# Performance work log

Hardware: AMD Instinct MI355X
Metric: run time of the kernel (lower is better)

The kernel has to match this reference:

```python
import jax, jax.numpy as jnp
import numpy as np

B, NPG, CIN, D, C, H, E, MAXN = 128, 1000, 16, 128, 12, 4, 640000, 1001
N = B * NPG
DH = D // H
NL = 3


def _ln(x, w, b):
    m = x.mean(-1, keepdims=True)
    v = ((x - m) ** 2).mean(-1, keepdims=True)
    return (x - m) * jax.lax.rsqrt(v + 1e-5) * w + b


def _mha(q_in, k_in, v_in, qkv_w, qkv_b, out_w, out_b, pad=None):
    # torch nn.MultiheadAttention with packed in_proj: rows [0:D]=Q, [D:2D]=K, [2D:3D]=V
    Tq, Tk = q_in.shape[1], k_in.shape[1]
    q = (q_in @ qkv_w[:D].T + qkv_b[:D]).reshape(-1, Tq, H, DH)
    k = (k_in @ qkv_w[D:2 * D].T + qkv_b[D:2 * D]).reshape(-1, Tk, H, DH)
    v = (v_in @ qkv_w[2 * D:].T + qkv_b[2 * D:]).reshape(-1, Tk, H, DH)
    s = jnp.einsum('bqhd,bkhd->bhqk', q, k) / np.sqrt(DH).astype(np.float32)
    if pad is not None:
        s = jnp.where(pad[:, None, None, :], jnp.float32(-1e30), s)
    a = jax.nn.softmax(s, axis=-1)
    o = jnp.einsum('bhqk,bkhd->bqhd', a, v).reshape(-1, Tq, D)
    return o @ out_w.T + out_b


def setup_inputs():
    key = jax.random.key(0)
    ks = iter(jax.random.split(key, 48))
    def nrm(shape, s=0.05):
        return jax.random.normal(next(ks), shape, jnp.float32) * s
    inp = {
        'x': nrm((N, CIN), 1.0),
        'edge_index': jax.random.randint(next(ks), (2, E), 0, N, dtype=jnp.int32),
        'batch': (jnp.arange(N, dtype=jnp.int32) // NPG),
        'in_w': nrm((D, CIN)), 'in_b': nrm((D,)),
        'gcn_w': nrm((NL, D, D)), 'gcn_b': nrm((NL, D)),
        'ln_w': jnp.ones((NL, D), jnp.float32), 'ln_b': jnp.zeros((NL, D), jnp.float32),
        'cq': nrm((C, D), 1.0),
        'sa_qkv_w': nrm((3 * D, D)), 'sa_qkv_b': nrm((3 * D,)),
        'sa_out_w': nrm((D, D)), 'sa_out_b': nrm((D,)),
        'ca_qkv_w': nrm((3 * D, D)), 'ca_qkv_b': nrm((3 * D,)),
        'ca_out_w': nrm((D, D)), 'ca_out_b': nrm((D,)),
        'n1_w': jnp.ones((D,), jnp.float32), 'n1_b': jnp.zeros((D,), jnp.float32),
        'n2_w': jnp.ones((D,), jnp.float32), 'n2_b': jnp.zeros((D,), jnp.float32),
        'n3_w': jnp.ones((D,), jnp.float32), 'n3_b': jnp.zeros((D,), jnp.float32),
        'ff1_w': nrm((4 * D, D)), 'ff1_b': nrm((4 * D,)),
        'ff2_w': nrm((D, 4 * D)), 'ff2_b': nrm((D,)),
        'op_ln_w': jnp.ones((D,), jnp.float32), 'op_ln_b': jnp.zeros((D,), jnp.float32),
        'op_w': nrm((1, D)), 'op_b': nrm((1,)),
    }
    return inp


def reference(x, edge_index, batch, in_w, in_b, gcn_w, gcn_b, ln_w, ln_b, cq,
              sa_qkv_w, sa_qkv_b, sa_out_w, sa_out_b,
              ca_qkv_w, ca_qkv_b, ca_out_w, ca_out_b,
              n1_w, n1_b, n2_w, n2_b, n3_w, n3_b,
              ff1_w, ff1_b, ff2_w, ff2_b, op_ln_w, op_ln_b, op_w, op_b):
    row, col = edge_index[0], edge_index[1]
    # ---- GCNBlock (eval mode: dropout = identity) ----
    h = x @ in_w.T + in_b  # input_proj since in_channels != hidden_dim
    # GCNConv normalization with self-loops (same for all layers)
    deg = jax.ops.segment_sum(jnp.ones((E,), h.dtype), col, num_segments=N) + 1.0
    dinv = jax.lax.rsqrt(deg)  # [N]
    en = dinv[row] * dinv[col]  # [E]
    self_w = (dinv * dinv)[:, None]
    residual = h
    for i in range(NL):
        hw = h @ gcn_w[i].T  # [N, D]
        agg = jax.ops.segment_sum(en[:, None] * hw[row], col, num_segments=N)
        agg = agg + self_w * hw + gcn_b[i]
        if i < NL - 1:
            h = jax.nn.relu(_ln(agg, ln_w[i], ln_b[i]))
            h = h + residual
            residual = h
        else:
            h = _ln(agg, ln_w[i], ln_b[i])
    # ---- pad variable-size graphs into dense memory + key padding mask ----
    counts = jax.ops.segment_sum(jnp.ones((N,), jnp.int32), batch, num_segments=B)
    starts = jnp.cumsum(counts) - counts
    pos = jnp.arange(N, dtype=jnp.int32) - starts[batch]
    memory = jnp.zeros((B, MAXN, D), h.dtype).at[batch, pos].set(h)
    pad = jnp.arange(MAXN)[None, :] >= counts[:, None]  # True = padded position
    # ---- TransformerDecoderLayer (norm_first=True), 1 layer ----
    t = jnp.broadcast_to(cq, (B, C, D))
    tn = _ln(t, n1_w, n1_b)
    t = t + _mha(tn, tn, tn, sa_qkv_w, sa_qkv_b, sa_out_w, sa_out_b)
    tn = _ln(t, n2_w, n2_b)
    t = t + _mha(tn, memory, memory, ca_qkv_w, ca_qkv_b, ca_out_w, ca_out_b, pad)
    tn = _ln(t, n3_w, n3_b)
    t = t + (jax.nn.relu(tn @ ff1_w.T + ff1_b) @ ff2_w.T + ff2_b)
    # ---- output projection: LN -> Linear(D,1) -> squeeze ----
    logits = (_ln(t, op_ln_w, op_ln_b) @ op_w.T + op_b)[..., 0]  # [B, C]
    return logits
```

## Files before the change

### kernel.cpp

```cpp
#include <hip/hip_runtime.h>
#include <hip/hip_bf16.h>

#define NNODES 128000
#define NEDGES 640000
#define BB 128
#define CC 12
#define DD 128
#define NROWS (BB*CC)
#define NSPLIT 8
#define CHUNK 125

typedef __attribute__((ext_vector_type(8))) short short8;
typedef __attribute__((ext_vector_type(4))) float f32x4;
typedef unsigned short ushort_t;

__device__ __forceinline__ unsigned pk2bf(float lo, float hi){
    union { __hip_bfloat162 h; unsigned u; } v;
    v.h = __float22bfloat162_rn(make_float2(lo, hi));
    return v.u;
}
__device__ __forceinline__ ushort_t f2bf(float f){
    union { __hip_bfloat16 h; ushort_t u; } v;
    v.h = __float2bfloat16(f);
    return v.u;
// ... 97 lines not shown
    int tid = threadIdx.x;
    int m0 = blockIdx.x*64;
    if (tid < 128){
        short8 z = {0,0,0,0,0,0,0,0};
        *(short8*)&xs[(tid>>1)*40 + 16 + (tid&1)*8] = z;
    }
    float4 xv = *(const float4*)(x + (size_t)m0*16 + tid*4);
    uint2 pk2;
    pk2.x = pk2bf(xv.x, xv.y);
    pk2.y = pk2bf(xv.z, xv.w);
    *(uint2*)&xs[(tid>>2)*40 + (tid&3)*4] = pk2;
    __syncthreads();
    int lane = tid & 63, w = tid >> 6;
    int lr = lane & 15, hi4 = lane >> 4, lk = hi4*8;
    short8 wf[8];
    #pragma unroll
    for (int nt=0; nt<8; ++nt)
        wf[nt] = *(const short8*)&Wpad[(nt*16 + lr)*32 + lk];
    short8 a = *(const short8*)&xs[(w*16 + lr)*40 + lk];
    f32x4 acc[8];
    #pragma unroll
    for (int nt=0; nt<8; ++nt)
        acc[nt] = __builtin_amdgcn_mfma_f32_16x16x32_bf16(wf[nt], a, (f32x4){0,0,0,0}, 0, 0, 0);
    size_t m = (size_t)m0 + w*16 + lr;
    #pragma unroll
    for (int nt=0; nt<8; ++nt){
        int n0 = nt*16 + hi4*4;
        float4 bv = *(const float4*)&bias[n0];
        uint2 pk;
        pk.x = pk2bf(acc[nt][0]+bv.x, acc[nt][1]+bv.y);
        pk.y = pk2bf(acc[nt][2]+bv.z, acc[nt][3]+bv.w);
        *(uint2*)&hbf[m*128 + n0] = pk;
    }
}

__global__ __launch_bounds__(256) void gemm_mfma(const ushort_t* __restrict__ A,
        const ushort_t* __restrict__ Wb, const float* __restrict__ bias, ushort_t* __restrict__ out){
    __shared__ __align__(16) ushort_t wl[128*136];
    int tid = threadIdx.x;
    #pragma unroll
    for (int i=0;i<8;++i){
        int elem = tid*8 + i*2048;
        int row = elem >> 7, k = elem & 127;
        *(short8*)&wl[row*136 + k] = *(const short8*)&Wb[elem];
    }
    __syncthreads();
    int lane = tid & 63, wave = tid >> 6;
    int m0 = blockIdx.x*128 + wave*32;
    int lr = lane & 15, hi4 = lane >> 4;
    int lk = hi4 * 8;
    f32x4 acc[2][8];
    #pragma unroll
    for (int t=0;t<2;++t)
        #pragma unroll
        for (int nt=0;nt<8;++nt) acc[t][nt] = (f32x4){0.f,0.f,0.f,0.f};
    const ushort_t* arow0 = A + (size_t)(m0 + lr)*128 + lk;
    const ushort_t* arow1 = arow0 + 16*128;
    #pragma unroll
    for (int kc=0; kc<4; ++kc){
        short8 h0 = *(const short8*)(arow0 + kc*32);
        short8 h1 = *(const short8*)(arow1 + kc*32);
        #pragma unroll
        for (int nt=0; nt<8; ++nt){
            short8 wf = *(const short8*)&wl[(nt*16 + lr)*136 + kc*32 + lk];
            acc[0][nt] = __builtin_amdgcn_mfma_f32_16x16x32_bf16(wf, h0, acc[0][nt], 0, 0, 0);
            acc[1][nt] = __builtin_amdgcn_mfma_f32_16x16x32_bf16(wf, h1, acc[1][nt], 0, 0, 0);
        }
    }
    #pragma unroll
    for (int nt=0; nt<8; ++nt){
        int n0 = nt*16 + hi4*4;
        float b0=0.f,b1=0.f,b2=0.f,b3=0.f;
        if (bias){
            float4 bv = *(const float4*)&bias[n0];
            b0=bv.x; b1=bv.y; b2=bv.z; b3=bv.w;
        }
        #pragma unroll
        for (int t=0; t<2; ++t){
            size_t m = (size_t)m0 + t*16 + lr;
            uint2 pk;
            pk.x = pk2bf(acc[t][nt][0]+b0, acc[t][nt][1]+b1);
            pk.y = pk2bf(acc[t][nt][2]+b2, acc[t][nt][3]+b3);
            *(uint2*)&out[m*128 + n0] = pk;
        }
    }
}

__global__ __launch_bounds__(256) void gcn_agg(ushort_t* __restrict__ hbf, const ushort_t* __restrict__ hwbf,
        const int* __restrict__ offs, const int2* __restrict__ ee,
        const float* __restrict__ dinv, const float* __restrict__ bias,
        const float* __restrict__ lnw, const float* __restrict__ lnb, int last){
    int wave = threadIdx.x >> 6;
    int lane = threadIdx.x & 63;
    int g = lane >> 4, sl = lane & 15;
    int node = blockIdx.x*16 + wave*4 + g;
    const uint4* hwu = (const uint4*)hwbf;
    uint4* hbu = (uint4*)hbf;
    uint4 sv = hwu[(size_t)node*16 + sl];
    uint4 rv = make_uint4(0,0,0,0);
    if (!last) rv = hbu[(size_t)node*16 + sl];
    float di = dinv[node];
    float sw = di*di;
    float a0 = sw*bfu_lo(sv.x), a1 = sw*bfu_hi(sv.x);
    float a2 = sw*bfu_lo(sv.y), a3 = sw*bfu_hi(sv.y);
    float a4 = sw*bfu_lo(sv.z), a5 = sw*bfu_hi(sv.z);
    float a6 = sw*bfu_lo(sv.w), a7 = sw*bfu_hi(sv.w);
    float b0=0,b1=0,b2=0,b3=0,b4=0,b5=0,b6=0,b7=0;
    int e0 = offs[node], e1 = offs[node+1];
    int e = e0;
    for (; e + 4 <= e1; e += 4){
        int2 p0 = ee[e], p1 = ee[e+1], p2 = ee[e+2], p3 = ee[e+3];
        uint4 u0 = hwu[(size_t)p0.x*16 + sl];
        uint4 u1 = hwu[(size_t)p1.x*16 + sl];
        uint4 u2 = hwu[(size_t)p2.x*16 + sl];
        uint4 u3 = hwu[(size_t)p3.x*16 + sl];
        float w0 = __int_as_float(p0.y), w1 = __int_as_float(p1.y);
        float w2 = __int_as_float(p2.y), w3 = __int_as_float(p3.y);
        a0 += w0*bfu_lo(u0.x); a1 += w0*bfu_hi(u0.x); a2 += w0*bfu_lo(u0.y); a3 += w0*bfu_hi(u0.y);
        a4 += w0*bfu_lo(u0.z); a5 += w0*bfu_hi(u0.z); a6 += w0*bfu_lo(u0.w); a7 += w0*bfu_hi(u0.w);
        b0 += w1*bfu_lo(u1.x); b1 += w1*bfu_hi(u1.x); b2 += w1*bfu_lo(u1.y); b3 += w1*bfu_hi(u1.y);
        b4 += w1*bfu_lo(u1.z); b5 += w1*bfu_hi(u1.z); b6 += w1*bfu_lo(u1.w); b7 += w1*bfu_hi(u1.w);
        a0 += w2*bfu_lo(u2.x); a1 += w2*bfu_hi(u2.x); a2 += w2*bfu_lo(u2.y); a3 += w2*bfu_hi(u2.y);
        a4 += w2*bfu_lo(u2.z); a5 += w2*bfu_hi(u2.z); a6 += w2*bfu_lo(u2.w); a7 += w2*bfu_hi(u2.w);
        b0 += w3*bfu_lo(u3.x); b1 += w3*bfu_hi(u3.x); b2 += w3*bfu_lo(u3.y); b3 += w3*bfu_hi(u3.y);
        b4 += w3*bfu_lo(u3.z); b5 += w3*bfu_hi(u3.z); b6 += w3*bfu_lo(u3.w); b7 += w3*bfu_hi(u3.w);
    }
    if (e + 2 <= e1){
        int2 p0 = ee[e], p1 = ee[e+1];
        uint4 u0 = hwu[(size_t)p0.x*16 + sl];
        uint4 u1 = hwu[(size_t)p1.x*16 + sl];
        float w0 = __int_as_float(p0.y), w1 = __int_as_float(p1.y);
        a0 += w0*bfu_lo(u0.x); a1 += w0*bfu_hi(u0.x); a2 += w0*bfu_lo(u0.y); a3 += w0*bfu_hi(u0.y);
        a4 += w0*bfu_lo(u0.z); a5 += w0*bfu_hi(u0.z); a6 += w0*bfu_lo(u0.w); a7 += w0*bfu_hi(u0.w);
        b0 += w1*bfu_lo(u1.x); b1 += w1*bfu_hi(u1.x); b2 += w1*bfu_lo(u1.y); b3 += w1*bfu_hi(u1.y);
        b4 += w1*bfu_lo(u1.z); b5 += w1*bfu_hi(u1.z); b6 += w1*bfu_lo(u1.w); b7 += w1*bfu_hi(u1.w);
        e += 2;
    }
    if (e < e1){
        int2 p0 = ee[e];
        uint4 u0 = hwu[(size_t)p0.x*16 + sl];
        float w0 = __int_as_float(p0.y);
        a0 += w0*bfu_lo(u0.x); a1 += w0*bfu_hi(u0.x); a2 += w0*bfu_lo(u0.y); a3 += w0*bfu_hi(u0.y);
        a4 += w0*bfu_lo(u0.z); a5 += w0*bfu_hi(u0.z); a6 += w0*bfu_lo(u0.w); a7 += w0*bfu_hi(u0.w);
    }
    a0 += b0; a1 += b1; a2 += b2; a3 += b3;
    a4 += b4; a5 += b5; a6 += b6; a7 += b7;
    {
        const float4* b4p = (const float4*)bias;
        float4 bb0 = b4p[sl*2], bb1 = b4p[sl*2+1];
        a0 += bb0.x; a1 += bb0.y; a2 += bb0.z; a3 += bb0.w;
        a4 += bb1.x; a5 += bb1.y; a6 += bb1.z; a7 += bb1.w;
    }
    float s = ((a0+a1)+(a2+a3))+((a4+a5)+(a6+a7));
    s += __shfl_xor(s,1); s += __shfl_xor(s,2); s += __shfl_xor(s,4); s += __shfl_xor(s,8);
    float mean = s*(1.f/128.f);
    a0 -= mean; a1 -= mean; a2 -= mean; a3 -= mean;
    a4 -= mean; a5 -= mean; a6 -= mean; a7 -= mean;
    float var = ((a0*a0+a1*a1)+(a2*a2+a3*a3))+((a4*a4+a5*a5)+(a6*a6+a7*a7));
    var += __shfl_xor(var,1); var += __shfl_xor(var,2); var += __shfl_xor(var,4); var += __shfl_xor(var,8);
    float rs = rsqrtf(var*(1.f/128.f) + 1e-5f);
    float4 w0v = ((const float4*)lnw)[sl*2], w1v = ((const float4*)lnw)[sl*2+1];
    float4 l0v = ((const float4*)lnb)[sl*2], l1v = ((const float4*)lnb)[sl*2+1];
    float y0 = a0*rs*w0v.x + l0v.x;
    float y1 = a1*rs*w0v.y + l0v.y;
    float y2 = a2*rs*w0v.z + l0v.z;
    float y3 = a3*rs*w0v.w + l0v.w;
    float y4 = a4*rs*w1v.x + l1v.x;
    float y5 = a5*rs*w1v.y + l1v.y;
    float y6 = a6*rs*w1v.z + l1v.z;
    float y7 = a7*rs*w1v.w + l1v.w;
    if (!last){
        y0 = fmaxf(y0,0.f) + bfu_lo(rv.x);
        y1 = fmaxf(y1,0.f) + bfu_hi(rv.x);
        y2 = fmaxf(y2,0.f) + bfu_lo(rv.y);
        y3 = fmaxf(y3,0.f) + bfu_hi(rv.y);
        y4 = fmaxf(y4,0.f) + bfu_lo(rv.z);
        y5 = fmaxf(y5,0.f) + bfu_hi(rv.z);
        y6 = fmaxf(y6,0.f) + bfu_lo(rv.w);
        y7 = fmaxf(y7,0.f) + bfu_hi(rv.w);
    }
    uint4 pk;
    pk.x = pk2bf(y0, y1);
    pk.y = pk2bf(y2, y3);
    pk.z = pk2bf(y4, y5);
    pk.w = pk2bf(y6, y7);
    hbu[(size_t)node*16 + sl] = pk;
}

__global__ __launch_bounds__(256) void dec_gemm(const ushort_t* __restrict__ A,
        const ushort_t* __restrict__ Wb, const float* __restrict__ bias,
        float* __restrict__ out, ushort_t* __restrict__ outbf,
        int K, int NO, int flags){
    int lane = threadIdx.x & 63, wave = threadIdx.x >> 6;
    int m0 = blockIdx.x*64 + wave*16;
    int n0 = blockIdx.y*128;
    int lr = lane & 15, lk = (lane>>4)*8;
    f32x4 acc[8];
    #pragma unroll
    for (int nt=0; nt<8; ++nt) acc[nt] = (f32x4){0.f,0.f,0.f,0.f};
    for (int ko = 0; ko < K; ko += 128){
        short8 bfrag[4][8];
        #pragma unroll
        for (int nt=0; nt<8; ++nt)
            #pragma unroll
            for (int kc=0; kc<4; ++kc)
                bfrag[kc][nt] = *(const short8*)&Wb[(size_t)(n0 + nt*16 + lr)*K + ko + kc*32 + lk];
        const ushort_t* arow = A + (size_t)(m0 + lr)*K + ko + lk;
        #pragma unroll
        for (int kc=0; kc<4; ++kc){
            short8 a = *(const short8*)(arow + kc*32);
            #pragma unroll
            for (int nt=0; nt<8; ++nt)
                acc[nt] = __builtin_amdgcn_mfma_f32_16x16x32_bf16(a, bfrag[kc][nt], acc[nt], 0, 0, 0);
        }
    }
    int orow0 = m0 + (lane>>4)*4;
    #pragma unroll
    for (int nt=0; nt<8; ++nt){
        int col = n0 + nt*16 + lr;
        float bv = bias[col];
        #pragma unroll
        for (int r=0; r<4; ++r){
            size_t idx = (size_t)(orow0 + r)*NO + col;
            float val = acc[nt][r] + bv;
            if (flags & 2) val = fmaxf(val, 0.f);
            if (flags & 1) val += out[idx];
            if (flags & 8) out[idx] = val;
            if (flags & 4) outbf[idx] = f2bf(val);
        }
    }
}

__global__ __launch_bounds__(256) void ln_rows(const float* __restrict__ x, float* __restrict__ y,
        const float* __restrict__ w, const float* __restrict__ b){
    int r = blockIdx.x*4 + (threadIdx.x>>6);
    int lane = threadIdx.x & 63;
    const float2* x2 = (const float2*)(x + (size_t)r*128);
    float2 v = x2[lane];
    float s = v.x+v.y;
    for (int o=32;o>0;o>>=1) s += __shfl_xor(s,o);
    float mean = s*(1.f/128.f);
    float dx=v.x-mean, dy=v.y-mean;
    float var = dx*dx+dy*dy;
    for (int o=32;o>0;o>>=1) var += __shfl_xor(var,o);
    float rs = rsqrtf(var*(1.f/128.f) + 1e-5f);
    float2 w2=((const float2*)w)[lane], b2=((const float2*)b)[lane];
    ((float2*)(y + (size_t)r*128))[lane] = make_float2(dx*rs*w2.x+b2.x, dy*rs*w2.y+b2.y);
}

__global__ __launch_bounds__(256) void ln_rows_bf(const float* __restrict__ x, ushort_t* __restrict__ y,
        const float* __restrict__ w, const float* __restrict__ b){
    int r = blockIdx.x*4 + (threadIdx.x>>6);
    int lane = threadIdx.x & 63;
    const float2* x2 = (const float2*)(x + (size_t)r*128);
    float2 v = x2[lane];
    float s = v.x+v.y;
    for (int o=32;o>0;o>>=1) s += __shfl_xor(s,o);
    float mean = s*(1.f/128.f);
    float dx=v.x-mean, dy=v.y-mean;
    float var = dx*dx+dy*dy;
    for (int o=32;o>0;o>>=1) var += __shfl_xor(var,o);
    float rs = rsqrtf(var*(1.f/128.f) + 1e-5f);
    float2 w2=((const float2*)w)[lane], b2=((const float2*)b)[lane];
    float yx = dx*rs*w2.x+b2.x, yy = dy*rs*w2.y+b2.y;
    ((unsigned*)y)[(size_t)r*64 + lane] = pk2bf(yx, yy);
}

__global__ __launch_bounds__(256) void small_gemm(const float* __restrict__ x, const float* __restrict__ W,
        const float* __restrict__ bias, float* __restrict__ out, int R, int K, int NO, int flags){
    int idx = blockIdx.x*256 + threadIdx.x;
    if (idx >= R*NO) return;
    int r = idx / NO, n = idx - r*NO;
    const float4* xr = (const float4*)(x + (size_t)r*K);
    const float4* wr = (const float4*)(W + (size_t)n*K);
    float a = bias ? bias[n] : 0.0f;
    int K4 = K>>2;
    for (int k=0;k<K4;++k){
        float4 xv = xr[k], wv = wr[k];
        a += xv.x*wv.x + xv.y*wv.y + xv.z*wv.z + xv.w*wv.w;
    }
    if (flags & 2) a = fmaxf(a, 0.f);
    if (flags & 1) a += out[idx];
    out[idx] = a;
}

__global__ __launch_bounds__(256) void copy12(const float* __restrict__ cq, float* __restrict__ t12){
    int i = blockIdx.x*256 + threadIdx.x;
    t12[i] = cq[i];
}

__global__ __launch_bounds__(256) void bcast_t(const float* __restrict__ t12, float* __restrict__ t_full){
    int idx = blockIdx.x*256 + threadIdx.x;
    int r = idx >> 7;
    t_full[idx] = t12[(r % 12)*128 + (idx & 127)];
}

__global__ __launch_bounds__(64) void self_attn12(const float* __restrict__ qkv, float* __restrict__ out){
    int hh = blockIdx.x;
    int lane = threadIdx.x;
    __shared__ float q[12][32], k[12][32], v[12][32], sc[12][12];
    for (int idx = lane; idx < 12*32; idx += 64){
        int c = idx>>5, d = idx&31;
        size_t base = (size_t)c*384 + hh*32 + d;
        q[c][d] = qkv[base] * 0.17677669529663687f;
        k[c][d] = qkv[base+128];
        v[c][d] = qkv[base+256];
    }
    __syncthreads();
    for (int p = lane; p < 144; p += 64){
        int qi = p/12, ki = p%12;
        float a = 0;
        #pragma unroll
        for (int d=0; d<32; ++d) a += q[qi][d]*k[ki][d];
        sc[qi][ki] = a;
    }
    __syncthreads();
    if (lane < 12){
        float m = -1e30f;
        for (int j=0;j<12;++j) m = fmaxf(m, sc[lane][j]);
        float sum=0;
        for (int j=0;j<12;++j){ float e=__expf(sc[lane][j]-m); sc[lane][j]=e; sum+=e; }
        float inv=1.f/sum;
        for (int j=0;j<12;++j) sc[lane][j]*=inv;
    }
    __syncthreads();
    for (int p = lane; p < 384; p += 64){
        int c = p>>5, d = p&31;
        float a=0;
        #pragma unroll
        for (int j=0;j<12;++j) a += sc[c][j]*v[j][d];
        out[(size_t)c*128 + hh*32 + d] = a;
    }
}

__global__ __launch_bounds__(512) void cross_attn_part(const float* __restrict__ q12,
        const ushort_t* __restrict__ K, const ushort_t* __restrict__ V,
        float* __restrict__ opart, float2* __restrict__ mlpart){
    __shared__ __align__(16) ushort_t qs[16*136];
    __shared__ __align__(16) unsigned char uni[128*136*2];
    __shared__ __align__(16) ushort_t pbf[4*16*136];
    __shared__ float2 ml[48];
    float* s32 = (float*)uni;
    ushort_t* vt = (ushort_t*)uni;

    int tid = threadIdx.x;
    int b = blockIdx.x / NSPLIT, sp = blockIdx.x % NSPLIT;
    int k0 = sp * CHUNK;
    int lane = tid & 63, w = tid >> 6;
    int lr = lane & 15, hi8 = (lane >> 4) * 8;

    const unsigned* Vu = (const unsigned*)V + ((size_t)b*1000 + k0)*64;
    unsigned vreg[16];
    #pragma unroll
    for (int j=0;j<15;++j) vreg[j] = Vu[tid + j*512];
    if (tid < 320) vreg[15] = Vu[tid + 7680];

    for (int i = tid; i < 16*128; i += 512){
        int r = i >> 7, c = i & 127;
        ushort_t v = 0;
        if (r < 12) v = f2bf(q12[r*128 + c] * 0.17677669529663687f);
        qs[r*136 + c] = v;
    }
    for (int i = tid; i < 4352; i += 512) ((unsigned*)pbf)[i] = 0;
    __syncthreads();

    {
        int krow = k0 + w*16 + lr; if (krow > k0 + 124) krow = k0 + 124;
        const ushort_t* Krow = K + ((size_t)b*1000 + krow)*128 + hi8;
        #pragma unroll
        for (int h=0; h<4; ++h){
            short8 kf = *(const short8*)(Krow + h*32);
            short8 qf = *(const short8*)&qs[lr*136 + h*32 + hi8];
            f32x4 d = __builtin_amdgcn_mfma_f32_16x16x32_bf16(qf, kf, (f32x4){0,0,0,0}, 0, 0, 0);
            int qbase = (lane>>4)*4;
            #pragma unroll
            for (int r=0; r<4; ++r){
                int qq = qbase + r;
                if (qq < 12) s32[(h*12+qq)*130 + w*16 + lr] = d[r];
            }
        }
    }
    __syncthreads();

    if (tid < 192){
        int hq = tid >> 2, sub = tid & 3;
        int h = hq / 12, qq = hq - h*12;
        float m = -1e30f;
        for (int kk = sub; kk < CHUNK; kk += 4) m = fmaxf(m, s32[hq*130 + kk]);
        m = fmaxf(m, __shfl_xor(m, 1));
        m = fmaxf(m, __shfl_xor(m, 2));
        float l = 0.f;
        for (int kk = sub; kk < CHUNK; kk += 4){
            float e = __expf(s32[hq*130 + kk] - m);
            l += e;
            pbf[(h*16+qq)*136 + kk] = f2bf(e);
        }
        l += __shfl_xor(l, 1);
        l += __shfl_xor(l, 2);
        if (sub == 0) ml[hq] = make_float2(m, l);
    }
    __syncthreads();

    #pragma unroll
    for (int j=0;j<15;++j){
        int i = tid + j*512;
        int kk = i >> 6, dp = (i & 63)*2;
        unsigned u = vreg[j];
        vt[dp*136 + kk]     = (ushort_t)(u & 0xFFFF);
        vt[(dp+1)*136 + kk] = (ushort_t)(u >> 16);
    }
    if (tid < 320){
        int i = tid + 7680;
        int kk = i >> 6, dp = (i & 63)*2;
        unsigned u = vreg[15];
        vt[dp*136 + kk]     = (ushort_t)(u & 0xFFFF);
        vt[(dp+1)*136 + kk] = (ushort_t)(u >> 16);
    }
    if (tid < 384){
        int dp = tid / 3, kk = 125 + tid % 3;
        vt[dp*136 + kk] = 0;
    }
    __syncthreads();

    {
        int h = w >> 1;
        f32x4 acc = (f32x4){0,0,0,0};
        #pragma unroll
        for (int kc=0; kc<4; ++kc){
            short8 pf = *(const short8*)&pbf[(h*16+lr)*136 + kc*32 + hi8];
            short8 vf = *(const short8*)&vt[(w*16+lr)*136 + kc*32 + hi8];
            acc = __builtin_amdgcn_mfma_f32_16x16x32_bf16(pf, vf, acc, 0, 0, 0);
        }
        int qbase = (lane>>4)*4;
        float* ob = opart + ((size_t)(b*NSPLIT+sp)*12)*128;
        #pragma unroll
        for (int r=0; r<4; ++r){
            int qq = qbase + r;
            if (qq < 12) ob[(size_t)qq*128 + w*16 + lr] = acc[r];
        }
    }
    if (tid < 48) mlpart[(size_t)(b*NSPLIT+sp)*48 + tid] = ml[tid];
}

__global__ __launch_bounds__(256) void cross_attn_comb(const float* __restrict__ opart,
        const float* __restrict__ mlpart, ushort_t* __restrict__ attbf){
    int b = blockIdx.x, tid = threadIdx.x;
    __shared__ float mls[NSPLIT*48*2];
    for (int i = tid; i < NSPLIT*48*2; i += 256) mls[i] = mlpart[(size_t)b*NSPLIT*96 + i];
    __syncthreads();
    for (int p = tid; p < 1536; p += 256){
        int qq = p >> 7, dp = p & 127, h = dp >> 5, hq = h*12 + qq;
        float M = -1e30f;
        #pragma unroll
        for (int sp=0; sp<NSPLIT; ++sp) M = fmaxf(M, mls[sp*96 + hq*2]);
        float L = 0.f, O = 0.f;
        #pragma unroll
        for (int sp=0; sp<NSPLIT; ++sp){
            float wgt = __expf(mls[sp*96 + hq*2] - M);
            L += wgt * mls[sp*96 + hq*2 + 1];
            O += wgt * opart[((size_t)(b*NSPLIT+sp)*12 + qq)*128 + dp];
        }
        attbf[((size_t)b*12 + qq)*128 + dp] = f2bf(O / L);
    }
}

__global__ __launch_bounds__(256) void final_out(const float* __restrict__ t,
        const float* __restrict__ lw, const float* __restrict__ lb,
        const float* __restrict__ ow, const float* __restrict__ ob, float* __restrict__ out){
    int r = blockIdx.x*4 + (threadIdx.x>>6);
    int lane = threadIdx.x & 63;
    const float2* x2 = (const float2*)(t + (size_t)r*128);
    float2 v = x2[lane];
    float s = v.x+v.y;
    for (int o=32;o>0;o>>=1) s += __shfl_xor(s,o);
    float mean = s*(1.f/128.f);
    float dx=v.x-mean, dy=v.y-mean;
    float var = dx*dx+dy*dy;
    for (int o=32;o>0;o>>=1) var += __shfl_xor(var,o);
    float rs = rsqrtf(var*(1.f/128.f)+1e-5f);
    float2 w2=((const float2*)lw)[lane], b2=((const float2*)lb)[lane];
    float2 o2=((const float2*)ow)[lane];
    float d = (dx*rs*w2.x+b2.x)*o2.x + (dy*rs*w2.y+b2.y)*o2.y;
    for (int o=32;o>0;o>>=1) d += __shfl_xor(d,o);
    if (lane==0) out[r] = d + ob[0];
}

extern "C" void kernel_launch(void* const* d_in, const int* in_sizes, int n_in,
                              void* d_out, int out_size, void* d_ws, size_t ws_size,
                              hipStream_t stream){
    (void)in_sizes; (void)n_in; (void)out_size; (void)ws_size;
    const float* x        = (const float*)d_in[0];
    const int*   eidx     = (const int*)d_in[1];
    const float* in_w     = (const float*)d_in[3];
    const float* in_b     = (const float*)d_in[4];
    const float* gcn_w    = (const float*)d_in[5];
    const float* gcn_b    = (const float*)d_in[6];
    const float* ln_w     = (const float*)d_in[7];
    const float* ln_b     = (const float*)d_in[8];
    const float* cq       = (const float*)d_in[9];
    const float* sa_qkv_w = (const float*)d_in[10];
    const float* sa_qkv_b = (const float*)d_in[11];
    const float* sa_out_w = (const float*)d_in[12];
    const float* sa_out_b = (const float*)d_in[13];
    const float* ca_qkv_w = (const float*)d_in[14];
    const float* ca_qkv_b = (const float*)d_in[15];
    const float* ca_out_w = (const float*)d_in[16];
    const float* ca_out_b = (const float*)d_in[17];
    const float* n1w=(const float*)d_in[18]; const float* n1b=(const float*)d_in[19];
    const float* n2w=(const float*)d_in[20]; const float* n2b=(const float*)d_in[21];
    const float* n3w=(const float*)d_in[22]; const float* n3b=(const float*)d_in[23];
    const float* ff1w=(const float*)d_in[24]; const float* ff1b=(const float*)d_in[25];
    const float* ff2w=(const float*)d_in[26]; const float* ff2b=(const float*)d_in[27];
    const float* opln_w=(const float*)d_in[28]; const float* opln_b=(const float*)d_in[29];
    const float* opw=(const float*)d_in[30]; const float* opb=(const float*)d_in[31];
    float* out = (float*)d_out;

    char* base = (char*)d_ws;
    size_t off = 0;
    auto alloc = [&](size_t bytes)->void*{
        void* r = base + off; off += (bytes + 255) & ~(size_t)255; return r;
    };
    ushort_t* hbf   = (ushort_t*)alloc((size_t)NNODES*DD*2);
    ushort_t* kbf   = (ushort_t*)alloc((size_t)NNODES*DD*2);
    ushort_t* vbf   = (ushort_t*)alloc((size_t)NNODES*DD*2);
    ushort_t* Wb    = (ushort_t*)alloc((size_t)5*DD*DD*2);
    ushort_t* Wpad  = (ushort_t*)alloc((size_t)DD*32*2);
    ushort_t* Wdec  = (ushort_t*)alloc((size_t)147456*2);
    float*    dinv  = (float*)alloc((size_t)NNODES*4);
    int*      cnt   = (int*)  alloc((size_t)NNODES*4);
    int*      offs  = (int*)  alloc((size_t)(NNODES+1)*4);
    int*      bsum  = (int*)  alloc(512*4);
    int2*     ee    = (int2*) alloc((size_t)NEDGES*8);
    float*    t12   = (float*)alloc((size_t)12*DD*4);
    float*    tn12  = (float*)alloc((size_t)12*DD*4);
    float*    sq12  = (float*)alloc((size_t)12*384*4);
    float*    att12 = (float*)alloc((size_t)12*DD*4);
    float*    q12   = (float*)alloc((size_t)12*DD*4);
    float*    tfull = (float*)alloc((size_t)NROWS*DD*4);
    ushort_t* tnbf  = (ushort_t*)alloc((size_t)NROWS*DD*2);
    ushort_t* attbf = (ushort_t*)alloc((size_t)NROWS*DD*2);
    ushort_t* ffhbf = (ushort_t*)alloc((size_t)NROWS*512*2);
    float*    opart = (float*)alloc((size_t)BB*NSPLIT*12*128*4);
    float2*   mlprt = (float2*)alloc((size_t)BB*NSPLIT*48*8);
    ushort_t* hwbf  = kbf;

    const int* erow = eidx;
    const int* ecol = eidx + NEDGES;

    hipMemsetAsync(cnt, 0, (size_t)NNODES*4, stream);
    count_edges<<<NEDGES/256, 256, 0, stream>>>(ecol, cnt);
    compute_dinv<<<NNODES/256, 256, 0, stream>>>(cnt, dinv);
    scan_a<<<NNODES/256, 256, 0, stream>>>(cnt, offs, bsum);
    scan_b<<<1, 512, 0, stream>>>(bsum, NNODES/256);
    scan_c<<<NNODES/256, 256, 0, stream>>>(offs, bsum);
    hipMemsetAsync(cnt, 0, (size_t)NNODES*4, stream);
    fill_csr<<<NEDGES/256, 256, 0, stream>>>(erow, ecol, offs, cnt, dinv, ee);

    conv_w<<<5*DD*DD/256, 256, 0, stream>>>(gcn_w, ca_qkv_w, Wb);
    conv_wpad<<<DD*32/256, 256, 0, stream>>>(in_w, Wpad);
    conv_wdec<<<576, 256, 0, stream>>>(ca_out_w, ff1w, ff2w, Wdec);

    in_proj_mfma<<<NNODES/64, 256, 0, stream>>>(x, Wpad, in_b, hbf);
    for (int i=0;i<3;++i){
        gemm_mfma<<<NNODES/128, 256, 0, stream>>>(hbf, Wb + (size_t)i*DD*DD, nullptr, hwbf);
        gcn_agg<<<NNODES/16, 256, 0, stream>>>(hbf, hwbf, offs, ee, dinv,
                gcn_b + (size_t)i*DD, ln_w + (size_t)i*DD, ln_b + (size_t)i*DD, i==2);
    }
    gemm_mfma<<<NNODES/128, 256, 0, stream>>>(hbf, Wb + (size_t)3*DD*DD, ca_qkv_b + DD,   kbf);
    gemm_mfma<<<NNODES/128, 256, 0, stream>>>(hbf, Wb + (size_t)4*DD*DD, ca_qkv_b + 2*DD, vbf);

    ln_rows<<<3, 256, 0, stream>>>(cq, tn12, n1w, n1b);
    small_gemm<<<18, 256, 0, stream>>>(tn12, sa_qkv_w, sa_qkv_b, sq12, 12, 128, 384, 0);
    self_attn12<<<4, 64, 0, stream>>>(sq12, att12);
    copy12<<<6, 256, 0, stream>>>(cq, t12);
    small_gemm<<<6, 256, 0, stream>>>(att12, sa_out_w, sa_out_b, t12, 12, 128, 128, 1);
    ln_rows<<<3, 256, 0, stream>>>(t12, tn12, n2w, n2b);
    small_gemm<<<6, 256, 0, stream>>>(tn12, ca_qkv_w, ca_qkv_b, q12, 12, 128, 128, 0);

    cross_attn_part<<<BB*NSPLIT, 512, 0, stream>>>(q12, kbf, vbf, opart, mlprt);
    cross_attn_comb<<<BB, 256, 0, stream>>>(opart, (const float*)mlprt, attbf);
    bcast_t<<<NROWS*DD/256, 256, 0, stream>>>(t12, tfull);
    dim3 g24_1(24,1), g24_4(24,4);
    dec_gemm<<<g24_1, 256, 0, stream>>>(attbf, Wdec, ca_out_b, tfull, nullptr, 128, 128, 1|8);
    ln_rows_bf<<<NROWS/4, 256, 0, stream>>>(tfull, tnbf, n3w, n3b);
    dec_gemm<<<g24_4, 256, 0, stream>>>(tnbf, Wdec + 16384, ff1b, nullptr, ffhbf, 128, 512, 2|4);
    dec_gemm<<<g24_1, 256, 0, stream>>>(ffhbf, Wdec + 81920, ff2b, tfull, nullptr, 512, 128, 1|8);
    final_out<<<NROWS/4, 256, 0, stream>>>(tfull, opln_w, opln_b, opw, opb, out);
}
```

Baseline: 428.4 us.

## Fuse K/V projections, collapse decoder prefix into one kernel, fold broadcast

Combines the K and V projection GEMMs into one kernel, so the node features are read once and each weight is staged through shared memory. Replaces the chain of small decoder-prefix launches (LN, self-attention QKV, attention, output projection, LN, query projection) with a single one-block kernel. Drops the broadcast kernel by adding the per-query residual inside the first decoder GEMM's epilogue. The goal is to cut launch overhead and one pass over the 128k-node activations. The cost is a serial single-block prefix and an extra barrier-separated phase in the KV kernel.

```diff
diff --git a/kernel.cpp b/kernel.cpp
--- a/kernel.cpp
+++ b/kernel.cpp
@@ -203,6 +203,99 @@
             pk.x = pk2bf(acc[t][nt][0]+b0, acc[t][nt][1]+b1);
             pk.y = pk2bf(acc[t][nt][2]+b2, acc[t][nt][3]+b3);
             *(uint2*)&out[m*128 + n0] = pk;
+        }
+    }
+}
+
+__global__ __launch_bounds__(256) void gemm_mfma_kv(const ushort_t* __restrict__ A,
+        const ushort_t* __restrict__ Wk, const ushort_t* __restrict__ Wv,
+        const float* __restrict__ bk, const float* __restrict__ bv,
+        ushort_t* __restrict__ outk, ushort_t* __restrict__ outv){
+    __shared__ __align__(16) ushort_t wl[128*136];
+    int tid = threadIdx.x;
+    int lane = tid & 63, wave = tid >> 6;
+    int m0 = blockIdx.x*128 + wave*32;
+    int lr = lane & 15, hi4 = lane >> 4;
+    int lk = hi4 * 8;
+    const ushort_t* arow0 = A + (size_t)(m0 + lr)*128 + lk;
+    const ushort_t* arow1 = arow0 + 16*128;
+    short8 h0[4], h1[4];
+    #pragma unroll
+    for (int kc=0;kc<4;++kc){
+        h0[kc] = *(const short8*)(arow0 + kc*32);
+        h1[kc] = *(const short8*)(arow1 + kc*32);
+    }
+    #pragma unroll
+    for (int i=0;i<8;++i){
+        int elem = tid*8 + i*2048;
+        int row = elem >> 7, k = elem & 127;
+        *(short8*)&wl[row*136 + k] = *(const short8*)&Wk[elem];
+    }
+    __syncthreads();
+    {
+        f32x4 acc[2][8];
+        #pragma unroll
+        for (int t=0;t<2;++t)
+            #pragma unroll
+            for (int nt=0;nt<8;++nt) acc[t][nt] = (f32x4){0.f,0.f,0.f,0.f};
+        #pragma unroll
+        for (int kc=0; kc<4; ++kc){
+            #pragma unroll
+            for (int nt=0; nt<8; ++nt){
+                short8 wf = *(const short8*)&wl[(nt*16 + lr)*136 + kc*32 + lk];
+                acc[0][nt] = __builtin_amdgcn_mfma_f32_16x16x32_bf16(wf, h0[kc], acc[0][nt], 0, 0, 0);
+                acc[1][nt] = __builtin_amdgcn_mfma_f32_16x16x32_bf16(wf, h1[kc], acc[1][nt], 0, 0, 0);
+            }
+        }
+        #pragma unroll
+        for (int nt=0; nt<8; ++nt){
+            int n0 = nt*16 + hi4*4;
+            float4 b4 = *(const float4*)&bk[n0];
+            #pragma unroll
+            for (int t=0; t<2; ++t){
+                size_t m = (size_t)m0 + t*16 + lr;
+                uint2 pk;
+                pk.x = pk2bf(acc[t][nt][0]+b4.x, acc[t][nt][1]+b4.y);
+                pk.y = pk2bf(acc[t][nt][2]+b4.z, acc[t][nt][3]+b4.w);
+                *(uint2*)&outk[m*128 + n0] = pk;
+            }
+        }
+    }
+    __syncthreads();
+    #pragma unroll
+    for (int i=0;i<8;++i){
+        int elem = tid*8 + i*2048;
+        int row = elem >> 7, k = elem & 127;
+        *(short8*)&wl[row*136 + k] = *(const short8*)&Wv[elem];
+    }
+    __syncthreads();
+    {
+        f32x4 acc[2][8];
+        #pragma unroll
+        for (int t=0;t<2;++t)
+            #pragma unroll
+            for (int nt=0;nt<8;++nt) acc[t][nt] = (f32x4){0.f,0.f,0.f,0.f};
+        #pragma unroll
+        for (int kc=0; kc<4; ++kc){
+            #pragma unroll
+            for (int nt=0; nt<8; ++nt){
+                short8 wf = *(const short8*)&wl[(nt*16 + lr)*136 + kc*32 + lk];
+                acc[0][nt] = __builtin_amdgcn_mfma_f32_16x16x32_bf16(wf, h0[kc], acc[0][nt], 0, 0, 0);
+                acc[1][nt] = __builtin_amdgcn_mfma_f32_16x16x32_bf16(wf, h1[kc], acc[1][nt], 0, 0, 0);
+            }
+        }
+        #pragma unroll
+        for (int nt=0; nt<8; ++nt){
+            int n0 = nt*16 + hi4*4;
+            float4 b4 = *(const float4*)&bv[n0];
+            #pragma unroll
+            for (int t=0; t<2; ++t){
+                size_t m = (size_t)m0 + t*16 + lr;
+                uint2 pk;
+                pk.x = pk2bf(acc[t][nt][0]+b4.x, acc[t][nt][1]+b4.y);
+                pk.y = pk2bf(acc[t][nt][2]+b4.z, acc[t][nt][3]+b4.w);
+                *(uint2*)&outv[m*128 + n0] = pk;
+            }
         }
     }
 }
@@ -311,6 +404,7 @@
 __global__ __launch_bounds__(256) void dec_gemm(const ushort_t* __restrict__ A,
         const ushort_t* __restrict__ Wb, const float* __restrict__ bias,
         float* __restrict__ out, ushort_t* __restrict__ outbf,
+        const float* __restrict__ tbc,
         int K, int NO, int flags){
     int lane = threadIdx.x & 63, wave = threadIdx.x >> 6;
     int m0 = blockIdx.x*64 + wave*16;
@@ -342,31 +436,259 @@
         float bv = bias[col];
         #pragma unroll
         for (int r=0; r<4; ++r){
-            size_t idx = (size_t)(orow0 + r)*NO + col;
+            int row = orow0 + r;
+            size_t idx = (size_t)row*NO + col;
             float val = acc[nt][r] + bv;
             if (flags & 2) val = fmaxf(val, 0.f);
             if (flags & 1) val += out[idx];
+            if (flags & 16) val += tbc[(row % 12)*128 + col];
             if (flags & 8) out[idx] = val;
             if (flags & 4) outbf[idx] = f2bf(val);
         }
     }
 }
 
-__global__ __launch_bounds__(256) void ln_rows(const float* __restrict__ x, float* __restrict__ y,
-        const float* __restrict__ w, const float* __restrict__ b){
-    int r = blockIdx.x*4 + (threadIdx.x>>6);
-    int lane = threadIdx.x & 63;
-    const float2* x2 = (const float2*)(x + (size_t)r*128);
-    float2 v = x2[lane];
-    float s = v.x+v.y;
-    for (int o=32;o>0;o>>=1) s += __shfl_xor(s,o);
-    float mean = s*(1.f/128.f);
-    float dx=v.x-mean, dy=v.y-mean;
-    float var = dx*dx+dy*dy;
-    for (int o=32;o>0;o>>=1) var += __shfl_xor(var,o);
-    float rs = rsqrtf(var*(1.f/128.f) + 1e-5f);
-    float2 w2=((const float2*)w)[lane], b2=((const float2*)b)[lane];
-    ((float2*)(y + (size_t)r*128))[lane] = make_float2(dx*rs*w2.x+b2.x, dy*rs*w2.y+b2.y);
+__global__ __launch_bounds__(256) void dec_prefix(const float* __restrict__ cq,
+        const float* __restrict__ sa_qkv_w, const float* __restrict__ sa_qkv_b,
+        const float* __restrict__ sa_out_w, const float* __restrict__ sa_out_b,
+        const float* __restrict__ ca_qkv_w, const float* __restrict__ ca_qkv_b,
+        const float* __restrict__ n1w, const float* __restrict__ n1b,
+        const float* __restrict__ n2w, const float* __restrict__ n2b,
+        float* __restrict__ t12, float* __restrict__ q12){
+    __shared__ float tn[12*128];
+    __shared__ float qkv[12*384];
+    __shared__ float att[12*128];
+    __shared__ float tt[12*128];
+    __shared__ float sc[4][12][12];
+    int tid = threadIdx.x;
+    int wave = tid >> 6, lane = tid & 63;
+    for (int r = wave; r < 12; r += 4){
+        float2 v = ((const float2*)(cq + r*128))[lane];
+        float s = v.x+v.y;
+        for (int o=32;o>0;o>>=1) s += __shfl_xor(s,o);
+        float mean = s*(1.f/128.f);
+        float dx=v.x-mean, dy=v.y-mean;
+        float var = dx*dx+dy*dy;
+        for (int o=32;o>0;o>>=1) var += __shfl_xor(var,o);
+        float rs = rsqrtf(var*(1.f/128.f)+1e-5f);
+        float2 w2=((const float2*)n1w)[lane], b2=((const float2*)n1b)[lane];
+        tn[r*128 + lane*2]   = dx*rs*w2.x+b2.x;
+        tn[r*128 + lane*2+1] = dy*rs*w2.y+b2.y;
+    }
+    __syncthreads();
+    for (int idx = tid; idx < 4608; idx += 256){
+        int r = idx / 384, n = idx - r*384;
+        const float4* xr = (const float4*)(tn + r*128);
+        const float4* wr = (const float4*)(sa_qkv_w + (size_t)n*128);
+        float a = sa_qkv_b[n];
+        #pragma unroll 8
+        for (int k=0;k<32;++k){
+            float4 xv = xr[k], wv = wr[k];
+            a += xv.x*wv.x + xv.y*wv.y + xv.z*wv.z + xv.w*wv.w;
+        }
+        qkv[idx] = a;
+    }
+    __syncthreads();
+    for (int p = tid; p < 576; p += 256){
+        int hh = p / 144, rem = p - hh*144, qi = rem/12, ki = rem - (rem/12)*12;
+        const float* qr = qkv + qi*384 + hh*32;
+        const float* kr = qkv + ki*384 + 128 + hh*32;
+        float a=0;
+        #pragma unroll
+        for (int d=0; d<32; ++d) a += qr[d]*kr[d];
+        sc[hh][qi][ki] = a * 0.17677669529663687f;
+    }
+    __syncthreads();
+    if (tid < 48){
+        int hh = tid/12, qi = tid - hh*12;
+        float m=-1e30f;
+        for (int j=0;j<12;++j) m = fmaxf(m, sc[hh][qi][j]);
+        float sum=0;
+        for (int j=0;j<12;++j){ float e=__expf(sc[hh][qi][j]-m); sc[hh][qi][j]=e; sum+=e; }
+        float inv=1.f/sum;
+        for (int j=0;j<12;++j) sc[hh][qi][j]*=inv;
+    }
+    __syncthreads();
+    for (int p = tid; p < 1536; p += 256){
+        int c = p>>7, d = p&127, hh = d>>5, dd = d&31;
+        float a=0;
+        #pragma unroll
+        for (int j=0;j<12;++j) a += sc[hh][c][j]*qkv[j*384+256+hh*32+dd];
+        att[p] = a;
+    }
+    __syncthreads();
+    for (int p = tid; p < 1536; p += 256){
+        int r = p>>7, n = p&127;
+        const float4* xr = (const float4*)(att + r*128);
+        const float4* wr = (const float4*)(sa_out_w + (size_t)n*128);
+        float a = sa_out_b[n];
+        #pragma unroll 8
+        for (int k=0;k<32;++k){
+            float4 xv = xr[k], wv = wr[k];
+            a += xv.x*wv.x + xv.y*wv.y + xv.z*wv.z + xv.w*wv.w;
+        }
+        float v = cq[p] + a;
+        tt[p] = v;
+        t12[p] = v;
+    }
+    __syncthreads();
+    for (int r = wave; r < 12; r += 4){
+        float2 v = ((const float2*)(tt + r*128))[lane];
+        float s = v.x+v.y;
+        for (int o=32;o>0;o>>=1) s += __shfl_xor(s,o);
+        float mean = s*(1.f/128.f);
+        float dx=v.x-mean, dy=v.y-mean;
+        float var = dx*dx+dy*dy;
+        for (int o=32;o>0;o>>=1) var += __shfl_xor(var,o);
+        float rs = rsqrtf(var*(1.f/128.f)+1e-5f);
+        float2 w2=((const float2*)n2w)[lane], b2=((const float2*)n2b)[lane];
+        tn[r*128 + lane*2]   = dx*rs*w2.x+b2.x;
+        tn[r*128 + lane*2+1] = dy*rs*w2.y+b2.y;
+    }
+    __syncthreads();
+    for (int p = tid; p < 1536; p += 256){
+        int r = p>>7, n = p&127;
+        const float4* xr = (const float4*)(tn + r*128);
+        const float4* wr = (const float4*)(ca_qkv_w + (size_t)n*128);
+        float a = ca_qkv_b[n];
+        #pragma unroll 8
+        for (int k=0;k<32;++k){
+            float4 xv = xr[k], wv = wr[k];
+            a += xv.x*wv.x + xv.y*wv.y + xv.z*wv.z + xv.w*wv.w;
+        }
+        q12[p] = a;
+    }
+}
+
+__global__ __launch_bounds__(512) void cross_attn_part(const float* __restrict__ q12,
+        const ushort_t* __restrict__ K, const ushort_t* __restrict__ V,
+        float* __restrict__ opart, float2* __restrict__ mlpart){
+    __shared__ __align__(16) ushort_t qs[16*136];
+    __shared__ __align__(16) unsigned char uni[128*136*2];
+    __shared__ __align__(16) ushort_t pbf[4*16*136];
+    __shared__ float2 ml[48];
+    float* s32 = (float*)uni;
+    ushort_t* vt = (ushort_t*)uni;
+
+    int tid = threadIdx.x;
+    int b = blockIdx.x / NSPLIT, sp = blockIdx.x % NSPLIT;
+    int k0 = sp * CHUNK;
+    int lane = tid & 63, w = tid >> 6;
+    int lr = lane & 15, hi8 = (lane >> 4) * 8;
+
+    const unsigned* Vu = (const unsigned*)V + ((size_t)b*1000 + k0)*64;
+    unsigned vreg[16];
+    #pragma unroll
+    for (int j=0;j<15;++j) vreg[j] = Vu[tid + j*512];
+    if (tid < 320) vreg[15] = Vu[tid + 7680];
+
+    for (int i = tid; i < 16*128; i += 512){
+        int r = i >> 7, c = i & 127;
+        ushort_t v = 0;
+        if (r < 12) v = f2bf(q12[r*128 + c] * 0.17677669529663687f);
+        qs[r*136 + c] = v;
+    }
+    for (int i = tid; i < 4352; i += 512) ((unsigned*)pbf)[i] = 0;
+    __syncthreads();
+
+    {
+        int krow = k0 + w*16 + lr; if (krow > k0 + 124) krow = k0 + 124;
+        const ushort_t* Krow = K + ((size_t)b*1000 + krow)*128 + hi8;
+        #pragma unroll
+        for (int h=0; h<4; ++h){
+            short8 kf = *(const short8*)(Krow + h*32);
+            short8 qf = *(const short8*)&qs[lr*136 + h*32 + hi8];
+            f32x4 d = __builtin_amdgcn_mfma_f32_16x16x32_bf16(qf, kf, (f32x4){0,0,0,0}, 0, 0, 0);
+            int qbase = (lane>>4)*4;
+            #pragma unroll
+            for (int r=0; r<4; ++r){
+                int qq = qbase + r;
+                if (qq < 12) s32[(h*12+qq)*130 + w*16 + lr] = d[r];
+            }
+        }
+    }
+    __syncthreads();
+
+    if (tid < 192){
+        int hq = tid >> 2, sub = tid & 3;
+        int h = hq / 12, qq = hq - h*12;
+        float m = -1e30f;
+        for (int kk = sub; kk < CHUNK; kk += 4) m = fmaxf(m, s32[hq*130 + kk]);
+        m = fmaxf(m, __shfl_xor(m, 1));
+        m = fmaxf(m, __shfl_xor(m, 2));
+        float l = 0.f;
+        for (int kk = sub; kk < CHUNK; kk += 4){
+            float e = __expf(s32[hq*130 + kk] - m);
+            l += e;
+            pbf[(h*16+qq)*136 + kk] = f2bf(e);
+        }
+        l += __shfl_xor(l, 1);
+        l += __shfl_xor(l, 2);
+        if (sub == 0) ml[hq] = make_float2(m, l);
+    }
+    __syncthreads();
+
+    #pragma unroll
+    for (int j=0;j<15;++j){
+        int i = tid + j*512;
+        int kk = i >> 6, dp = (i & 63)*2;
+        unsigned u = vreg[j];
+        vt[dp*136 + kk]     = (ushort_t)(u & 0xFFFF);
+        vt[(dp+1)*136 + kk] = (ushort_t)(u >> 16);
+    }
+    if (tid < 320){
+        int i = tid + 7680;
+        int kk = i >> 6, dp = (i & 63)*2;
+        unsigned u = vreg[15];
+        vt[dp*136 + kk]     = (ushort_t)(u & 0xFFFF);
+        vt[(dp+1)*136 + kk] = (ushort_t)(u >> 16);
+    }
+    if (tid < 384){
+        int dp = tid / 3, kk = 125 + tid % 3;
+        vt[dp*136 + kk] = 0;
+    }
+    __syncthreads();
+
+    {
+        int h = w >> 1;
+        f32x4 acc = (f32x4){0,0,0,0};
+        #pragma unroll
+        for (int kc=0; kc<4; ++kc){
+            short8 pf = *(const short8*)&pbf[(h*16+lr)*136 + kc*32 + hi8];
+            short8 vf = *(const short8*)&vt[(w*16+lr)*136 + kc*32 + hi8];
+            acc = __builtin_amdgcn_mfma_f32_16x16x32_bf16(pf, vf, acc, 0, 0, 0);
+        }
+        int qbase = (lane>>4)*4;
+        float* ob = opart + ((size_t)(b*NSPLIT+sp)*12)*128;
+        #pragma unroll
+        for (int r=0; r<4; ++r){
+            int qq = qbase + r;
+            if (qq < 12) ob[(size_t)qq*128 + w*16 + lr] = acc[r];
+        }
+    }
+    if (tid < 48) mlpart[(size_t)(b*NSPLIT+sp)*48 + tid] = ml[tid];
+}
+
+__global__ __launch_bounds__(256) void cross_attn_comb(const float* __restrict__ opart,
+        const float* __restrict__ mlpart, ushort_t* __restrict__ attbf){
+    int b = blockIdx.x, tid = threadIdx.x;
+    __shared__ float mls[NSPLIT*48*2];
+    for (int i = tid; i < NSPLIT*48*2; i += 256) mls[i] = mlpart[(size_t)b*NSPLIT*96 + i];
+    __syncthreads();
+    for (int p = tid; p < 1536; p += 256){
+        int qq = p >> 7, dp = p & 127, h = dp >> 5, hq = h*12 + qq;
+        float M = -1e30f;
+        #pragma unroll
+        for (int sp=0; sp<NSPLIT; ++sp) M = fmaxf(M, mls[sp*96 + hq*2]);
+        float L = 0.f, O = 0.f;
+        #pragma unroll
+        for (int sp=0; sp<NSPLIT; ++sp){
+            float wgt = __expf(mls[sp*96 + hq*2] - M);
+            L += wgt * mls[sp*96 + hq*2 + 1];
+            O += wgt * opart[((size_t)(b*NSPLIT+sp)*12 + qq)*128 + dp];
+        }
+        attbf[((size_t)b*12 + qq)*128 + dp] = f2bf(O / L);
+    }
 }
 
 __global__ __launch_bounds__(256) void ln_rows_bf(const float* __restrict__ x, ushort_t* __restrict__ y,
@@ -385,204 +707,6 @@
     float2 w2=((const float2*)w)[lane], b2=((const float2*)b)[lane];
     float yx = dx*rs*w2.x+b2.x, yy = dy*rs*w2.y+b2.y;
     ((unsigned*)y)[(size_t)r*64 + lane] = pk2bf(yx, yy);
-}
-
-__global__ __launch_bounds__(256) void small_gemm(const float* __restrict__ x, const float* __restrict__ W,
-        const float* __restrict__ bias, float* __restrict__ out, int R, int K, int NO, int flags){
-    int idx = blockIdx.x*256 + threadIdx.x;
-    if (idx >= R*NO) return;
-    int r = idx / NO, n = idx - r*NO;
-    const float4* xr = (const float4*)(x + (size_t)r*K);
-    const float4* wr = (const float4*)(W + (size_t)n*K);
-    float a = bias ? bias[n] : 0.0f;
-    int K4 = K>>2;
-    for (int k=0;k<K4;++k){
-        float4 xv = xr[k], wv = wr[k];
-        a += xv.x*wv.x + xv.y*wv.y + xv.z*wv.z + xv.w*wv.w;
-    }
-    if (flags & 2) a = fmaxf(a, 0.f);
-    if (flags & 1) a += out[idx];
-    out[idx] = a;
-}
-
-__global__ __launch_bounds__(256) void copy12(const float* __restrict__ cq, float* __restrict__ t12){
-    int i = blockIdx.x*256 + threadIdx.x;
-    t12[i] = cq[i];
-}
-
-__global__ __launch_bounds__(256) void bcast_t(const float* __restrict__ t12, float* __restrict__ t_full){
-    int idx = blockIdx.x*256 + threadIdx.x;
-    int r = idx >> 7;
-    t_full[idx] = t12[(r % 12)*128 + (idx & 127)];
-}
-
-__global__ __launch_bounds__(64) void self_attn12(const float* __restrict__ qkv, float* __restrict__ out){
-    int hh = blockIdx.x;
-    int lane = threadIdx.x;
-    __shared__ float q[12][32], k[12][32], v[12][32], sc[12][12];
-    for (int idx = lane; idx < 12*32; idx += 64){
-        int c = idx>>5, d = idx&31;
-        size_t base = (size_t)c*384 + hh*32 + d;
-        q[c][d] = qkv[base] * 0.17677669529663687f;
-        k[c][d] = qkv[base+128];
-        v[c][d] = qkv[base+256];
-    }
-    __syncthreads();
-    for (int p = lane; p < 144; p += 64){
-        int qi = p/12, ki = p%12;
-        float a = 0;
-        #pragma unroll
-        for (int d=0; d<32; ++d) a += q[qi][d]*k[ki][d];
-        sc[qi][ki] = a;
-    }
-    __syncthreads();
-    if (lane < 12){
-        float m = -1e30f;
-        for (int j=0;j<12;++j) m = fmaxf(m, sc[lane][j]);
-        float sum=0;
-        for (int j=0;j<12;++j){ float e=__expf(sc[lane][j]-m); sc[lane][j]=e; sum+=e; }
-        float inv=1.f/sum;
-        for (int j=0;j<12;++j) sc[lane][j]*=inv;
-    }
-    __syncthreads();
-    for (int p = lane; p < 384; p += 64){
-        int c = p>>5, d = p&31;
-        float a=0;
-        #pragma unroll
-        for (int j=0;j<12;++j) a += sc[c][j]*v[j][d];
-        out[(size_t)c*128 + hh*32 + d] = a;
-    }
-}
-
-__global__ __launch_bounds__(512) void cross_attn_part(const float* __restrict__ q12,
-        const ushort_t* __restrict__ K, const ushort_t* __restrict__ V,
-        float* __restrict__ opart, float2* __restrict__ mlpart){
-    __shared__ __align__(16) ushort_t qs[16*136];
-    __shared__ __align__(16) unsigned char uni[128*136*2];
-    __shared__ __align__(16) ushort_t pbf[4*16*136];
-    __shared__ float2 ml[48];
-    float* s32 = (float*)uni;
-    ushort_t* vt = (ushort_t*)uni;
-
-    int tid = threadIdx.x;
-    int b = blockIdx.x / NSPLIT, sp = blockIdx.x % NSPLIT;
-    int k0 = sp * CHUNK;
-    int lane = tid & 63, w = tid >> 6;
-    int lr = lane & 15, hi8 = (lane >> 4) * 8;
-
-    const unsigned* Vu = (const unsigned*)V + ((size_t)b*1000 + k0)*64;
-    unsigned vreg[16];
-    #pragma unroll
-    for (int j=0;j<15;++j) vreg[j] = Vu[tid + j*512];
-    if (tid < 320) vreg[15] = Vu[tid + 7680];
-
-    for (int i = tid; i < 16*128; i += 512){
-        int r = i >> 7, c = i & 127;
-        ushort_t v = 0;
-        if (r < 12) v = f2bf(q12[r*128 + c] * 0.17677669529663687f);
-        qs[r*136 + c] = v;
-    }
-    for (int i = tid; i < 4352; i += 512) ((unsigned*)pbf)[i] = 0;
-    __syncthreads();
-
-    {
-        int krow = k0 + w*16 + lr; if (krow > k0 + 124) krow = k0 + 124;
-        const ushort_t* Krow = K + ((size_t)b*1000 + krow)*128 + hi8;
-        #pragma unroll
-        for (int h=0; h<4; ++h){
-            short8 kf = *(const short8*)(Krow + h*32);
-            short8 qf = *(const short8*)&qs[lr*136 + h*32 + hi8];
-            f32x4 d = __builtin_amdgcn_mfma_f32_16x16x32_bf16(qf, kf, (f32x4){0,0,0,0}, 0, 0, 0);
-            int qbase = (lane>>4)*4;
-            #pragma unroll
-            for (int r=0; r<4; ++r){
-                int qq = qbase + r;
-                if (qq < 12) s32[(h*12+qq)*130 + w*16 + lr] = d[r];
-            }
-        }
-    }
-    __syncthreads();
-
-    if (tid < 192){
-        int hq = tid >> 2, sub = tid & 3;
-        int h = hq / 12, qq = hq - h*12;
-        float m = -1e30f;
-        for (int kk = sub; kk < CHUNK; kk += 4) m = fmaxf(m, s32[hq*130 + kk]);
-        m = fmaxf(m, __shfl_xor(m, 1));
-        m = fmaxf(m, __shfl_xor(m, 2));
-        float l = 0.f;
-        for (int kk = sub; kk < CHUNK; kk += 4){
-            float e = __expf(s32[hq*130 + kk] - m);
-            l += e;
-            pbf[(h*16+qq)*136 + kk] = f2bf(e);
-        }
-        l += __shfl_xor(l, 1);
-        l += __shfl_xor(l, 2);
-        if (sub == 0) ml[hq] = make_float2(m, l);
-    }
-    __syncthreads();
-
-    #pragma unroll
-    for (int j=0;j<15;++j){
-        int i = tid + j*512;
-        int kk = i >> 6, dp = (i & 63)*2;
-        unsigned u = vreg[j];
-        vt[dp*136 + kk]     = (ushort_t)(u & 0xFFFF);
-        vt[(dp+1)*136 + kk] = (ushort_t)(u >> 16);
-    }
-    if (tid < 320){
-        int i = tid + 7680;
-        int kk = i >> 6, dp = (i & 63)*2;
-        unsigned u = vreg[15];
-        vt[dp*136 + kk]     = (ushort_t)(u & 0xFFFF);
-        vt[(dp+1)*136 + kk] = (ushort_t)(u >> 16);
-    }
-    if (tid < 384){
-        int dp = tid / 3, kk = 125 + tid % 3;
-        vt[dp*136 + kk] = 0;
-    }
-    __syncthreads();
-
-    {
-        int h = w >> 1;
-        f32x4 acc = (f32x4){0,0,0,0};
-        #pragma unroll
-        for (int kc=0; kc<4; ++kc){
-            short8 pf = *(const short8*)&pbf[(h*16+lr)*136 + kc*32 + hi8];
-            short8 vf = *(const short8*)&vt[(w*16+lr)*136 + kc*32 + hi8];
-            acc = __builtin_amdgcn_mfma_f32_16x16x32_bf16(pf, vf, acc, 0, 0, 0);
-        }
-        int qbase = (lane>>4)*4;
-        float* ob = opart + ((size_t)(b*NSPLIT+sp)*12)*128;
-        #pragma unroll
-        for (int r=0; r<4; ++r){
-            int qq = qbase + r;
-            if (qq < 12) ob[(size_t)qq*128 + w*16 + lr] = acc[r];
-        }
-    }
-    if (tid < 48) mlpart[(size_t)(b*NSPLIT+sp)*48 + tid] = ml[tid];
-}
-
-__global__ __launch_bounds__(256) void cross_attn_comb(const float* __restrict__ opart,
-        const float* __restrict__ mlpart, ushort_t* __restrict__ attbf){
-    int b = blockIdx.x, tid = threadIdx.x;
-    __shared__ float mls[NSPLIT*48*2];
-    for (int i = tid; i < NSPLIT*48*2; i += 256) mls[i] = mlpart[(size_t)b*NSPLIT*96 + i];
-    __syncthreads();
-    for (int p = tid; p < 1536; p += 256){
-        int qq = p >> 7, dp = p & 127, h = dp >> 5, hq = h*12 + qq;
-        float M = -1e30f;
-        #pragma unroll
-        for (int sp=0; sp<NSPLIT; ++sp) M = fmaxf(M, mls[sp*96 + hq*2]);
-        float L = 0.f, O = 0.f;
-        #pragma unroll
-        for (int sp=0; sp<NSPLIT; ++sp){
-            float wgt = __expf(mls[sp*96 + hq*2] - M);
-            L += wgt * mls[sp*96 + hq*2 + 1];
-            O += wgt * opart[((size_t)(b*NSPLIT+sp)*12 + qq)*128 + dp];
-        }
-        attbf[((size_t)b*12 + qq)*128 + dp] = f2bf(O / L);
-    }
 }
 
 __global__ __launch_bounds__(256) void final_out(const float* __restrict__ t,
@@ -653,9 +777,6 @@
     int*      bsum  = (int*)  alloc(512*4);
     int2*     ee    = (int2*) alloc((size_t)NEDGES*8);
     float*    t12   = (float*)alloc((size_t)12*DD*4);
-    float*    tn12  = (float*)alloc((size_t)12*DD*4);
-    float*    sq12  = (float*)alloc((size_t)12*384*4);
-    float*    att12 = (float*)alloc((size_t)12*DD*4);
     float*    q12   = (float*)alloc((size_t)12*DD*4);
     float*    tfull = (float*)alloc((size_t)NROWS*DD*4);
     ushort_t* tnbf  = (ushort_t*)alloc((size_t)NROWS*DD*2);
@@ -687,24 +808,18 @@
         gcn_agg<<<NNODES/16, 256, 0, stream>>>(hbf, hwbf, offs, ee, dinv,
                 gcn_b + (size_t)i*DD, ln_w + (size_t)i*DD, ln_b + (size_t)i*DD, i==2);
     }
-    gemm_mfma<<<NNODES/128, 256, 0, stream>>>(hbf, Wb + (size_t)3*DD*DD, ca_qkv_b + DD,   kbf);
-    gemm_mfma<<<NNODES/128, 256, 0, stream>>>(hbf, Wb + (size_t)4*DD*DD, ca_qkv_b + 2*DD, vbf);
-
-    ln_rows<<<3, 256, 0, stream>>>(cq, tn12, n1w, n1b);
-    small_gemm<<<18, 256, 0, stream>>>(tn12, sa_qkv_w, sa_qkv_b, sq12, 12, 128, 384, 0);
-    self_attn12<<<4, 64, 0, stream>>>(sq12, att12);
-    copy12<<<6, 256, 0, stream>>>(cq, t12);
-    small_gemm<<<6, 256, 0, stream>>>(att12, sa_out_w, sa_out_b, t12, 12, 128, 128, 1);
-    ln_rows<<<3, 256, 0, stream>>>(t12, tn12, n2w, n2b);
-    small_gemm<<<6, 256, 0, stream>>>(tn12, ca_qkv_w, ca_qkv_b, q12, 12, 128, 128, 0);
+    gemm_mfma_kv<<<NNODES/128, 256, 0, stream>>>(hbf, Wb + (size_t)3*DD*DD, Wb + (size_t)4*DD*DD,
+            ca_qkv_b + DD, ca_qkv_b + 2*DD, kbf, vbf);
+
+    dec_prefix<<<1, 256, 0, stream>>>(cq, sa_qkv_w, sa_qkv_b, sa_out_w, sa_out_b,
+            ca_qkv_w, ca_qkv_b, n1w, n1b, n2w, n2b, t12, q12);
 
     cross_attn_part<<<BB*NSPLIT, 512, 0, stream>>>(q12, kbf, vbf, opart, mlprt);
     cross_attn_comb<<<BB, 256, 0, stream>>>(opart, (const float*)mlprt, attbf);
-    bcast_t<<<NROWS*DD/256, 256, 0, stream>>>(t12, tfull);
     dim3 g24_1(24,1), g24_4(24,4);
-    dec_gemm<<<g24_1, 256, 0, stream>>>(attbf, Wdec, ca_out_b, tfull, nullptr, 128, 128, 1|8);
+    dec_gemm<<<g24_1, 256, 0, stream>>>(attbf, Wdec, ca_out_b, tfull, nullptr, t12, 128, 128, 16|8);
     ln_rows_bf<<<NROWS/4, 256, 0, stream>>>(tfull, tnbf, n3w, n3b);
-    dec_gemm<<<g24_4, 256, 0, stream>>>(tnbf, Wdec + 16384, ff1b, nullptr, ffhbf, 128, 512, 2|4);
-    dec_gemm<<<g24_1, 256, 0, stream>>>(ffhbf, Wdec + 81920, ff2b, tfull, nullptr, 512, 128, 1|8);
+    dec_gemm<<<g24_4, 256, 0, stream>>>(tnbf, Wdec + 16384, ff1b, nullptr, ffhbf, nullptr, 128, 512, 2|4);
+    dec_gemm<<<g24_1, 256, 0, stream>>>(ffhbf, Wdec + 81920, ff2b, tfull, nullptr, nullptr, 512, 128, 1|8);
     final_out<<<NROWS/4, 256, 0, stream>>>(tfull, opln_w, opln_b, opw, opb, out);
 }
```

Measured after the change: 510.3 us. +19.1%, slower.
